# Kernel optimization log

Measured on AMD Instinct MI355X. Metric: run time of the kernel, lower is better.

The kernel has to match this reference:

```python
import jax, jax.numpy as jnp
import numpy as np

N, E, D, H, HD, DFF = 2048, 32768, 256, 8, 32, 1024
NEG = -1e30  # masked-out logit (exp -> 0 in fp32)


def _layer_norm(x, w, b, eps=1e-5):
    mu = jnp.mean(x, axis=-1, keepdims=True)
    var = jnp.mean((x - mu) ** 2, axis=-1, keepdims=True)
    return (x - mu) * jax.lax.rsqrt(var + eps) * w + b


def setup_inputs() -> dict:
    key = jax.random.key(0)
    ks = jax.random.split(key, 24)
    w = lambda k, shape: (jax.random.normal(k, shape, dtype=jnp.float32) * 0.02)
    inp = {
        "node_feat": jax.random.normal(ks[0], (N, D), dtype=jnp.float32),
        "edge_feat": jax.random.normal(ks[1], (E, 10), dtype=jnp.float32),
        "src": jax.random.randint(ks[2], (E,), 0, N),
        "dst": jax.random.randint(ks[3], (E,), 0, N),
        "Wq": w(ks[4], (D, D)), "bq": jnp.zeros((D,), jnp.float32),
        "Wk": w(ks[5], (D, D)), "bk": jnp.zeros((D,), jnp.float32),
        "Wv": w(ks[6], (D, D)), "bv": jnp.zeros((D,), jnp.float32),
        "Wo": w(ks[7], (D, D)), "bo": jnp.zeros((D,), jnp.float32),
        "We": w(ks[8], (10, H)), "be": jnp.zeros((H,), jnp.float32),
        "n1w": jnp.ones((D,), jnp.float32), "n1b": jnp.zeros((D,), jnp.float32),
        "W1": w(ks[9], (D, DFF)), "b1": jnp.zeros((DFF,), jnp.float32),
        "W2": w(ks[10], (DFF, D)), "b2": jnp.zeros((D,), jnp.float32),
        "n2w": jnp.ones((D,), jnp.float32), "n2b": jnp.zeros((D,), jnp.float32),
    }
    return inp


def reference(node_feat, edge_feat, src, dst, Wq, bq, Wk, bk, Wv, bv, Wo, bo,
              We, be, n1w, n1b, W1, b1, W2, b2, n2w, n2b):
    n = node_feat.shape[0]
    Q = (node_feat @ Wq + bq).reshape(n, H, HD)
    K = (node_feat @ Wk + bk).reshape(n, H, HD)
    V = (node_feat @ Wv + bv).reshape(n, H, HD)

    # dense [n, n, H] scores (faithful to the original dense blowup)
    scores = jnp.einsum('ihd,jhd->ijh', Q, K) / np.sqrt(HD).astype(np.float32)

    # scatter edge bias into dense matrix (last-write semantics like torch indexing)
    edge_bias = edge_feat @ We + be                       # [E, H]
    bias = jnp.zeros((n, n, H), jnp.float32).at[src, dst].set(edge_bias)
    scores = scores + bias

    # symmetric adjacency mask with self-loops
    adj = jnp.zeros((n, n), jnp.float32)
    adj = adj.at[src, dst].set(1.0).at[dst, src].set(1.0)
    idx = jnp.arange(n)
    adj = adj.at[idx, idx].set(1.0)

    scores = jnp.where(adj[:, :, None] > 0, scores, NEG)
    attn = jax.nn.softmax(scores, axis=1)                 # softmax over j (dim=1)

    out = jnp.einsum('ijh,jhd->ihd', attn, V).reshape(n, D)
    out = out @ Wo + bo
    out = _layer_norm(out + node_feat, n1w, n1b)
    ffn = jax.nn.relu(out @ W1 + b1) @ W2 + b2
    out = _layer_norm(out + ffn, n2w, n2b)
    return out
```

## Files before the change

### kernel.cpp

```cpp
#include <hip/hip_runtime.h>
#include <hip/hip_bf16.h>

#define NN 2048
#define E_CNT 32768
#define D 256
#define DFF 1024
#define MAXN 256
#define NCONV 14

typedef __hip_bfloat16 bf16;
typedef __attribute__((ext_vector_type(8))) short short8;
typedef __attribute__((ext_vector_type(4))) float f32x4;

__device__ __forceinline__ short bf2s(bf16 x) { union { bf16 b; short s; } u; u.b = x; return u.s; }
__device__ __forceinline__ float bs2f(unsigned short v) { return __uint_as_float(((unsigned)v) << 16); }

struct ConvTab { const void* src[NCONV]; int n[NCONV]; int off[NCONV]; };
struct TransTab { const void* src[6]; int K[6]; int N[6]; int off[6]; };

__global__ __launch_bounds__(256) void k_sniff(const unsigned short* __restrict__ p,
                                               int* __restrict__ flagp)
{
    int tid = threadIdx.x;
    int cnt = 0;
    for (int t = tid; t < 2048; t += 256) {
        float f = __uint_as_float(((unsigned)p[t]) << 16);
        if (!(fabsf(f) < 1000.f)) cnt++;
    }
#pragma unroll
    for (int off = 32; off > 0; off >>= 1) cnt += __shfl_down(cnt, off, 64);
    __shared__ int s[4];
    if ((tid & 63) == 0) s[tid >> 6] = cnt;
    __syncthreads();
    if (tid == 0) *flagp = (s[0] + s[1] + s[2] + s[3] > 64) ? 1 : 0;
}

__global__ __launch_bounds__(256) void k_convert(ConvTab tab, float* __restrict__ base,
                                                 bf16* __restrict__ nb,
                                                 const void* __restrict__ nodesrc,
                                                 const int* __restrict__ flagp)
{
    int a = blockIdx.y;
    int flag = *flagp;
    int idx0 = blockIdx.x * 2048 + threadIdx.x;
    if (a == NCONV) {
        const int n = NN * D;
        if (flag) {
            const float* s = (const float*)nodesrc;
#pragma unroll
            for (int k = 0; k < 8; k++) { int i = idx0 + k * 256; if (i < n) nb[i] = __float2bfloat16(s[i]); }
        } else {
            const short* s = (const short*)nodesrc;
            short* d = (short*)nb;
#pragma unroll
            for (int k = 0; k < 8; k++) { int i = idx0 + k * 256; if (i < n) d[i] = s[i]; }
        }
        return;
    }
    int n = tab.n[a];
    const void* s = tab.src[a];
    float* d = base + tab.off[a];
    if (flag) {
        const float* sf = (const float*)s;
#pragma unroll
        for (int k = 0; k < 8; k++) { int i = idx0 + k * 256; if (i < n) d[i] = sf[i]; }
    } else {
        const bf16* sb = (const bf16*)s;
#pragma unroll
        for (int k = 0; k < 8; k++) { int i = idx0 + k * 256; if (i < n) d[i] = __bfloat162float(sb[i]); }
    }
}

__global__ __launch_bounds__(256) void k_trans(TransTab tab, short* __restrict__ wt,
                                               const int* __restrict__ flagp)
{
    int a = blockIdx.z;
    int Kd = tab.K[a], Nd = tab.N[a];
    int n0 = blockIdx.x * 32, k0 = blockIdx.y * 32;
    if (n0 >= Nd || k0 >= Kd) return;
    int flag = *flagp;
    __shared__ short tile[32][33];
    int t = threadIdx.x, c = t & 31, r4 = t >> 5;
    const void* s = tab.src[a];
#pragma unroll
    for (int p = 0; p < 4; p++) {
        int r = r4 + p * 8;
        short v;
        if (flag) v = bf2s(__float2bfloat16(((const float*)s)[(size_t)(k0 + r) * Nd + n0 + c]));
        else      v = ((const short*)s)[(size_t)(k0 + r) * Nd + n0 + c];
        tile[r][c] = v;
    }
    __syncthreads();
    short* dT = wt + tab.off[a];
#pragma unroll
    for (int p = 0; p < 4; p++) {
        int r = r4 + p * 8;
        dT[(size_t)(n0 + r) * Kd + k0 + c] = tile[c][r];
    }
}

__global__ __launch_bounds__(256) void k_fill_edge(
    const int* __restrict__ src, const int* __restrict__ dst,
    int* __restrict__ pair, unsigned* __restrict__ bits,
    const float* __restrict__ ef, const float* __restrict__ We,
    const float* __restrict__ be, float* __restrict__ ebuf)
{
    __shared__ float w[80], bb[8];
    int tid = threadIdx.x;
    int e = blockIdx.x * 256 + tid;
    if (blockIdx.y == 0) {
        if (e < E_CNT) {
            int s = src[e], d = dst[e];
            atomicMax(&pair[(size_t)s * NN + d], e);
            atomicOr(&bits[s * 64 + (d >> 5)], 1u << (d & 31));
            atomicOr(&bits[d * 64 + (s >> 5)], 1u << (s & 31));
        }
        if (e < NN) atomicOr(&bits[e * 64 + (e >> 5)], 1u << (e & 31));
        return;
    }
    if (tid < 80) w[tid] = We[tid];
    if (tid < 8)  bb[tid] = be[tid];
    __syncthreads();
    if (e < E_CNT) {
        float v[10];
#pragma unroll
        for (int t2 = 0; t2 < 10; t2++) v[t2] = ef[e * 10 + t2];
#pragma unroll
        for (int h = 0; h < 8; h++) {
            float s = bb[h];
#pragma unroll
            for (int t2 = 0; t2 < 10; t2++) s += v[t2] * w[t2 * 8 + h];
            ebuf[e * 8 + h] = s;
        }
    }
}

__global__ __launch_bounds__(256) void k_qkv3(
    const bf16* __restrict__ A,
    const bf16* __restrict__ WqT, const bf16* __restrict__ WkT, const bf16* __restrict__ WvT,
    const float* __restrict__ bq, const float* __restrict__ bk, const float* __restrict__ bv,
    float* __restrict__ Qo, bf16* __restrict__ Kb, bf16* __restrict__ Vb)
{
    int z = blockIdx.z;
    const bf16* BT = (z == 0) ? WqT : (z == 1) ? WkT : WvT;
    const float* bias = (z == 0) ? bq : (z == 1) ? bk : bv;
    __shared__ __align__(16) short As[2][4 * 64 * 8];
    __shared__ __align__(16) short Bs[2][4 * 32 * 8];
    int t = threadIdx.x, w = t >> 6, l = t & 63, fr = l & 15, fc = l >> 4;
    int i0 = blockIdx.x * 64, j0 = blockIdx.y * 32;
    int lr = t >> 2, lc = t & 3;
    f32x4 acc0 = {0.f, 0.f, 0.f, 0.f}, acc1 = {0.f, 0.f, 0.f, 0.f};
    const short* ap = (const short*)A + (size_t)(i0 + lr) * D + lc * 8;
    const short* bp = (const short*)BT + (size_t)(j0 + (lr & 31)) * D + lc * 8;
    for (int k0 = 0; k0 < D; k0 += 64) {
        short8 av0 = *(const short8*)(ap + k0);
        short8 av1 = *(const short8*)(ap + k0 + 32);
        short8 bv0 = {}, bv1 = {};
        if (t < 128) {
            bv0 = *(const short8*)(bp + k0);
            bv1 = *(const short8*)(bp + k0 + 32);
        }
        __syncthreads();
        *(short8*)&As[0][(lc * 64 + lr) * 8] = av0;
        *(short8*)&As[1][(lc * 64 + lr) * 8] = av1;
        if (t < 128) {
            *(short8*)&Bs[0][(lc * 32 + lr) * 8] = bv0;
            *(short8*)&Bs[1][(lc * 32 + lr) * 8] = bv1;
        }
        __syncthreads();
#pragma unroll
        for (int s = 0; s < 2; s++) {
            short8 af  = *(const short8*)&As[s][(fc * 64 + w * 16 + fr) * 8];
            short8 bf0 = *(const short8*)&Bs[s][(fc * 32 + fr) * 8];
            short8 bf1 = *(const short8*)&Bs[s][(fc * 32 + 16 + fr) * 8];
            acc0 = __builtin_amdgcn_mfma_f32_16x16x32_bf16(af, bf0, acc0, 0, 0, 0);
            acc1 = __builtin_amdgcn_mfma_f32_16x16x32_bf16(af, bf1, acc1, 0, 0, 0);
        }
    }
    float bb0 = bias[j0 + fr], bb1 = bias[j0 + 16 + fr];
    int orow = i0 + w * 16 + fc * 4;
    if (z == 0) {
#pragma unroll
        for (int j = 0; j < 4; j++) {
            Qo[(size_t)(orow + j) * D + j0 + fr]      = acc0[j] + bb0;
            Qo[(size_t)(orow + j) * D + j0 + 16 + fr] = acc1[j] + bb1;
        }
    } else {
        bf16* C = (z == 1) ? Kb : Vb;
#pragma unroll
        for (int j = 0; j < 4; j++) {
            C[(size_t)(orow + j) * D + j0 + fr]      = __float2bfloat16(acc0[j] + bb0);
            C[(size_t)(orow + j) * D + j0 + 16 + fr] = __float2bfloat16(acc1[j] + bb1);
        }
    }
}

template<int EPI>
__global__ __launch_bounds__(256) void k_gemm(
    const bf16* __restrict__ A, const bf16* __restrict__ BT,
    const float* __restrict__ bias, void* __restrict__ Cp, int N, int K)
{
    __shared__ __align__(16) short As[2][4 * 64 * 8];
    __shared__ __align__(16) short Bs[2][4 * 32 * 8];
    int t = threadIdx.x;
    int w = t >> 6, l = t & 63;
    int fr = l & 15, fc = l >> 4;
    int i0 = blockIdx.x * 64, j0 = blockIdx.y * 32;
    int lr = t >> 2, lc = t & 3;
    f32x4 acc0 = {0.f, 0.f, 0.f, 0.f}, acc1 = {0.f, 0.f, 0.f, 0.f};
    const short* ap = (const short*)A + (size_t)(i0 + lr) * K + lc * 8;
    const short* bp = (const short*)BT + (size_t)(j0 + (lr & 31)) * K + lc * 8;
    for (int k0 = 0; k0 < K; k0 += 64) {
        short8 av0 = *(const short8*)(ap + k0);
        short8 av1 = *(const short8*)(ap + k0 + 32);
        short8 bv0 = {}, bv1 = {};
        if (t < 128) {
            bv0 = *(const short8*)(bp + k0);
            bv1 = *(const short8*)(bp + k0 + 32);
        }
        __syncthreads();
        *(short8*)&As[0][(lc * 64 + lr) * 8] = av0;
        *(short8*)&As[1][(lc * 64 + lr) * 8] = av1;
        if (t < 128) {
            *(short8*)&Bs[0][(lc * 32 + lr) * 8] = bv0;
            *(short8*)&Bs[1][(lc * 32 + lr) * 8] = bv1;
        }
        __syncthreads();
#pragma unroll
        for (int s = 0; s < 2; s++) {
            short8 af  = *(const short8*)&As[s][(fc * 64 + w * 16 + fr) * 8];
            short8 bf0 = *(const short8*)&Bs[s][(fc * 32 + fr) * 8];
            short8 bf1 = *(const short8*)&Bs[s][(fc * 32 + 16 + fr) * 8];
            acc0 = __builtin_amdgcn_mfma_f32_16x16x32_bf16(af, bf0, acc0, 0, 0, 0);
            acc1 = __builtin_amdgcn_mfma_f32_16x16x32_bf16(af, bf1, acc1, 0, 0, 0);
        }
    }
    float bb0 = bias[j0 + fr];
    float bb1 = bias[j0 + 16 + fr];
    int orow = i0 + w * 16 + fc * 4;
    if (EPI == 0) {
        float* C = (float*)Cp;
#pragma unroll
        for (int j = 0; j < 4; j++) {
            C[(size_t)(orow + j) * N + j0 + fr]      = acc0[j] + bb0;
            C[(size_t)(orow + j) * N + j0 + 16 + fr] = acc1[j] + bb1;
        }
    } else {
        bf16* C = (bf16*)Cp;
#pragma unroll
        for (int j = 0; j < 4; j++) {
            C[(size_t)(orow + j) * N + j0 + fr]      = __float2bfloat16(fmaxf(acc0[j] + bb0, 0.f));
            C[(size_t)(orow + j) * N + j0 + 16 + fr] = __float2bfloat16(fmaxf(acc1[j] + bb1, 0.f));
        }
    }
}

__global__ __launch_bounds__(256) void k_attn(
    const float* __restrict__ Q, const bf16* __restrict__ K,
    const bf16* __restrict__ V, const float* __restrict__ eb,
    const int* __restrict__ pair, const unsigned* __restrict__ bits,
    bf16* __restrict__ attn_out)
{
    int i = blockIdx.x;
    int tid = threadIdx.x;
    __shared__ float q[D];
    __shared__ int   nbr[MAXN];
    __shared__ int   eid[MAXN];
    __shared__ float sc[MAXN][8];
    __shared__ float mh[8], lhi[8];
    __shared__ int   nn_s;
    q[tid] = Q[(size_t)i * D + tid];
    if (tid < 64) {
        unsigned wrd = bits[i * 64 + tid];
        int cnt = __popc(wrd);
        int pre = cnt;
#pragma unroll
        for (int off = 1; off < 64; off <<= 1) {
            int v = __shfl_up(pre, off, 64);
            if (tid >= off) pre += v;
        }
        int pos = pre - cnt;
        while (wrd) {
            int b = __ffs(wrd) - 1;
            wrd &= wrd - 1;
            if (pos < MAXN) nbr[pos] = tid * 32 + b;
            pos++;
        }
        if (tid == 63) nn_s = (pre < MAXN) ? pre : MAXN;
    }
    __syncthreads();
    int nn = nn_s;
    const size_t prow = (size_t)i * NN;
    for (int n = tid; n < nn; n += 256) eid[n] = pair[prow + nbr[n]];
    __syncthreads();
    const short* Ks = (const short*)K;
    for (int t2 = tid; t2 < nn * 8; t2 += 256) {
        int n = t2 >> 3, h = t2 & 7;
        int j = nbr[n];
        const short8* kr = (const short8*)(Ks + (size_t)j * D + h * 32);
        const float4* qr = (const float4*)(q + h * 32);
        float s = 0.f;
#pragma unroll
        for (int c = 0; c < 4; c++) {
            short8 kv = kr[c];
            float4 q0 = qr[c * 2], q1 = qr[c * 2 + 1];
            s += q0.x * bs2f((unsigned short)kv[0]) + q0.y * bs2f((unsigned short)kv[1])
               + q0.z * bs2f((unsigned short)kv[2]) + q0.w * bs2f((unsigned short)kv[3])
               + q1.x * bs2f((unsigned short)kv[4]) + q1.y * bs2f((unsigned short)kv[5])
               + q1.z * bs2f((unsigned short)kv[6]) + q1.w * bs2f((unsigned short)kv[7]);
        }
        s *= 0.17677669529663687f;
        int e = eid[n];
        if (e >= 0) s += eb[e * 8 + h];
        sc[n][h] = s;
    }
    __syncthreads();
    {
        int h = tid >> 5, l32 = tid & 31;
        float m = -1e30f;
        for (int n = l32; n < nn; n += 32) m = fmaxf(m, sc[n][h]);
#pragma unroll
        for (int off = 1; off < 32; off <<= 1) m = fmaxf(m, __shfl_xor(m, off, 64));
        float lsum = 0.f;
        for (int n = l32; n < nn; n += 32) lsum += __expf(sc[n][h] - m);
#pragma unroll
        for (int off = 1; off < 32; off <<= 1) lsum += __shfl_xor(lsum, off, 64);
        if (l32 == 0) { mh[h] = m; lhi[h] = 1.f / lsum; }
    }
    __syncthreads();
    for (int t2 = tid; t2 < nn * 8; t2 += 256) {
        int n = t2 >> 3, h = t2 & 7;
        sc[n][h] = __expf(sc[n][h] - mh[h]);
    }
    __syncthreads();
    int h = tid >> 5;
    const unsigned short* Vu = (const unsigned short*)V;
    float acc = 0.f;
    int n = 0;
    for (; n + 4 <= nn; n += 4) {
        int j0 = nbr[n], j1 = nbr[n + 1], j2 = nbr[n + 2], j3 = nbr[n + 3];
        float p0 = sc[n][h], p1 = sc[n + 1][h], p2 = sc[n + 2][h], p3 = sc[n + 3][h];
        acc += p0 * bs2f(Vu[(size_t)j0 * D + tid]) + p1 * bs2f(Vu[(size_t)j1 * D + tid])
             + p2 * bs2f(Vu[(size_t)j2 * D + tid]) + p3 * bs2f(Vu[(size_t)j3 * D + tid]);
    }
    for (; n < nn; n++) acc += sc[n][h] * bs2f(Vu[(size_t)nbr[n] * D + tid]);
    attn_out[(size_t)i * D + tid] = __float2bfloat16(acc * lhi[h]);
}

template<int MODE>
__global__ __launch_bounds__(256) void k_ln(
    const float* __restrict__ g, const float* __restrict__ res,
    const float* __restrict__ w, const float* __restrict__ b,
    float* __restrict__ xf, bf16* __restrict__ xb, const int* __restrict__ flagp)
{
    int row = blockIdx.x * 4 + (threadIdx.x >> 6);
    int l = threadIdx.x & 63;
    size_t base = (size_t)row * D + l * 4;
    float4 gv = *(const float4*)(g + base);
    float4 rv = *(const float4*)(res + base);
    float v0 = gv.x + rv.x, v1 = gv.y + rv.y, v2 = gv.z + rv.z, v3 = gv.w + rv.w;
    float s = v0 + v1 + v2 + v3;
    float q = v0 * v0 + v1 * v1 + v2 * v2 + v3 * v3;
#pragma unroll
    for (int off = 32; off > 0; off >>= 1) {
        s += __shfl_xor(s, off, 64);
        q += __shfl_xor(q, off, 64);
    }
    float mu  = s * (1.f / D);
    float var = q * (1.f / D) - mu * mu;
    float rs  = rsqrtf(var + 1e-5f);
    float4 wv = *(const float4*)(w + l * 4);
    float4 bv = *(const float4*)(b + l * 4);
    float o0 = (v0 - mu) * rs * wv.x + bv.x;
    float o1 = (v1 - mu) * rs * wv.y + bv.y;
    float o2 = (v2 - mu) * rs * wv.z + bv.z;
    float o3 = (v3 - mu) * rs * wv.w + bv.w;
    if (MODE == 0) {
        float4 o; o.x = o0; o.y = o1; o.z = o2; o.w = o3;
        *(float4*)(xf + base) = o;
        xb[base + 0] = __float2bfloat16(o0);
        xb[base + 1] = __float2bfloat16(o1);
        xb[base + 2] = __float2bfloat16(o2);
        xb[base + 3] = __float2bfloat16(o3);
    } else {
        if (*flagp) {
            float4 o; o.x = o0; o.y = o1; o.z = o2; o.w = o3;
            *(float4*)(xf + base) = o;
        } else {
            xb[base + 0] = __float2bfloat16(o0);
            xb[base + 1] = __float2bfloat16(o1);
            xb[base + 2] = __float2bfloat16(o2);
            xb[base + 3] = __float2bfloat16(o3);
        }
    }
}

extern "C" void kernel_launch(void* const* d_in, const int* in_sizes, int n_in,
                              void* d_out, int out_size, void* d_ws, size_t ws_size,
                              hipStream_t stream)
{
    (void)n_in; (void)out_size; (void)ws_size;
    const int* src = (const int*)d_in[2];
    const int* dst = (const int*)d_in[3];

    char* ws = (char*)d_ws;
    const size_t KB = 1024;
    float*    conv     = (float*)ws;
    bf16*     node_b16 = (bf16*)(ws + 3584 * KB);
    short*    wt       = (short*)(ws + 4608 * KB);
    int*      flagp    = (int*)(ws + 6144 * KB);
    unsigned* bits     = (unsigned*)(ws + 6272 * KB);
    float*    eb       = (float*)(ws + 7168 * KB);
    float*    Q        = (float*)(ws + 8192 * KB);
    bf16*     Kb       = (bf16*)(ws + 10240 * KB);
    bf16*     Vb       = (bf16*)(ws + 11264 * KB);
    bf16*     attn_out = (bf16*)(ws + 12288 * KB);
    float*    x1f      = (float*)(ws + 13312 * KB);
    bf16*     x1b      = (bf16*)(ws + 15360 * KB);
    int*      pair     = (int*)(ws + 16384 * KB);
    float*    g2       = (float*)(ws + 32768 * KB);
    bf16*     hid      = (bf16*)(ws + 34816 * KB);
    float*    g4       = (float*)(ws + 38912 * KB);

    static const int conv_idx[NCONV] = {0, 1, 5, 7, 9, 11, 12, 13, 14, 15, 17, 19, 20, 21};
    ConvTab tab;
    int off = 0;
    for (int a = 0; a < NCONV; a++) {
        int gi = conv_idx[a];
        tab.src[a] = d_in[gi];
        tab.n[a]   = in_sizes[gi];
        tab.off[a] = off;
        off += (in_sizes[gi] + 255) & ~255;
    }
    const float* node_f32 = conv + tab.off[0];
    const float* edge_f32 = conv + tab.off[1];
    const float* fbq  = conv + tab.off[2];
    const float* fbk  = conv + tab.off[3];
    const float* fbv  = conv + tab.off[4];
    const float* fbo  = conv + tab.off[5];
    const float* fWe  = conv + tab.off[6];
    const float* fbe  = conv + tab.off[7];
    const float* fn1w = conv + tab.off[8];
    const float* fn1b = conv + tab.off[9];
    const float* fb1  = conv + tab.off[10];
    const float* fb2  = conv + tab.off[11];
    const float* fn2w = conv + tab.off[12];
    const float* fn2b = conv + tab.off[13];

    TransTab tt;
    const int widx[6] = {4, 6, 8, 10, 16, 18};
    const int wK[6] = {256, 256, 256, 256, 256, 1024};
    const int wN[6] = {256, 256, 256, 256, 1024, 256};
    const int woff[6] = {0, 65536, 131072, 196608, 262144, 524288};
    for (int a = 0; a < 6; a++) { tt.src[a] = d_in[widx[a]]; tt.K[a] = wK[a]; tt.N[a] = wN[a]; tt.off[a] = woff[a]; }
    const bf16* WqT = (const bf16*)(wt + 0);
    const bf16* WkT = (const bf16*)(wt + 65536);
    const bf16* WvT = (const bf16*)(wt + 131072);
    const bf16* WoT = (const bf16*)(wt + 196608);
    const bf16* W1T = (const bf16*)(wt + 262144);
    const bf16* W2T = (const bf16*)(wt + 524288);

    hipMemsetAsync(bits, 0x00, (size_t)NN * 64 * 4, stream);
    hipMemsetAsync(pair, 0xFF, (size_t)NN * NN * 4, stream);

    k_sniff<<<1, 256, 0, stream>>>((const unsigned short*)d_in[0], flagp);
    k_convert<<<dim3(256, NCONV + 1), 256, 0, stream>>>(tab, conv, node_b16, d_in[0], flagp);
    k_trans<<<dim3(32, 32, 6), 256, 0, stream>>>(tt, wt, flagp);
    k_fill_edge<<<dim3(128, 2), 256, 0, stream>>>(src, dst, pair, bits,
                                                  edge_f32, fWe, fbe, eb);
    k_qkv3<<<dim3(32, 8, 3), 256, 0, stream>>>(node_b16, WqT, WkT, WvT, fbq, fbk, fbv, Q, Kb, Vb);
    k_attn<<<NN, 256, 0, stream>>>(Q, Kb, Vb, eb, pair, bits, attn_out);

    k_gemm<0><<<dim3(32, 8), 256, 0, stream>>>(attn_out, WoT, fbo, g2, D, D);
    k_ln<0><<<NN / 4, 256, 0, stream>>>(g2, node_f32, fn1w, fn1b, x1f, x1b, flagp);
    k_gemm<1><<<dim3(32, 32), 256, 0, stream>>>(x1b, W1T, fb1, hid, DFF, D);
    k_gemm<0><<<dim3(32, 8), 256, 0, stream>>>(hid, W2T, fb2, g4, D, DFF);
    k_ln<1><<<NN / 4, 256, 0, stream>>>(g4, x1f, fn2w, fn2b, (float*)d_out, (bf16*)d_out, flagp);
}
```

Before: 167.3 us.

## Merge prep kernels, fuse GEMM with LayerNorm, store Q in bf16

```diff
diff --git a/kernel.cpp b/kernel.cpp
--- a/kernel.cpp
+++ b/kernel.cpp
@@ -6,7 +6,6 @@
 #define D 256
 #define DFF 1024
 #define MAXN 256
-#define NCONV 14
 
 typedef __hip_bfloat16 bf16;
 typedef __attribute__((ext_vector_type(8))) short short8;
@@ -15,122 +14,145 @@
 __device__ __forceinline__ short bf2s(bf16 x) { union { bf16 b; short s; } u; u.b = x; return u.s; }
 __device__ __forceinline__ float bs2f(unsigned short v) { return __uint_as_float(((unsigned)v) << 16); }
 
-struct ConvTab { const void* src[NCONV]; int n[NCONV]; int off[NCONV]; };
-struct TransTab { const void* src[6]; int K[6]; int N[6]; int off[6]; };
-
-__global__ __launch_bounds__(256) void k_sniff(const unsigned short* __restrict__ p,
-                                               int* __restrict__ flagp)
+__device__ __forceinline__ int sniff_flag(const unsigned short* p, int* sh)
 {
     int tid = threadIdx.x;
     int cnt = 0;
-    for (int t = tid; t < 2048; t += 256) {
-        float f = __uint_as_float(((unsigned)p[t]) << 16);
+    for (int t = tid; t < 512; t += 256) {
+        float f = bs2f(p[t]);
         if (!(fabsf(f) < 1000.f)) cnt++;
     }
 #pragma unroll
     for (int off = 32; off > 0; off >>= 1) cnt += __shfl_down(cnt, off, 64);
-    __shared__ int s[4];
-    if ((tid & 63) == 0) s[tid >> 6] = cnt;
+    if ((tid & 63) == 0) sh[tid >> 6] = cnt;
     __syncthreads();
-    if (tid == 0) *flagp = (s[0] + s[1] + s[2] + s[3] > 64) ? 1 : 0;
-}
-
-__global__ __launch_bounds__(256) void k_convert(ConvTab tab, float* __restrict__ base,
-                                                 bf16* __restrict__ nb,
-                                                 const void* __restrict__ nodesrc,
-                                                 const int* __restrict__ flagp)
-{
-    int a = blockIdx.y;
-    int flag = *flagp;
-    int idx0 = blockIdx.x * 2048 + threadIdx.x;
-    if (a == NCONV) {
-        const int n = NN * D;
+    int tot = sh[0] + sh[1] + sh[2] + sh[3];
+    return tot > 16;
+}
+
+struct PrepArgs {
+    const void* node; const void* edge;
+    const int* src; const int* dst;
+    const void* We; const void* be;
+    const void* wsrc[6];
+    const void* ssrc[10]; int sn[10]; int soff[10];
+    bf16* node_b16; float* node_f32; float* smalls;
+    short* wt; float* eb; int* pair; unsigned* bits;
+    int* flagp;
+};
+
+__global__ __launch_bounds__(256) void k_prep(PrepArgs A)
+{
+    __shared__ int sh[4];
+    __shared__ short tile[32][33];
+    __shared__ float wsm[80], bbs[8];
+    const int b = blockIdx.x;
+    const int t = threadIdx.x;
+
+    if (b >= 1408 && b < 1536) {
+        int e = (b - 1408) * 256 + t;
+        if (e < E_CNT) {
+            int s = A.src[e], d = A.dst[e];
+            atomicMax(&A.pair[(size_t)s * NN + d], e);
+            atomicOr(&A.bits[s * 64 + (d >> 5)], 1u << (d & 31));
+            atomicOr(&A.bits[d * 64 + (s >> 5)], 1u << (s & 31));
+        }
+        int n = (b - 1408) * 16 + (t >> 4);
+        if (t < 128 && n < NN) atomicOr(&A.bits[n * 64 + (n >> 5)], 1u << (n & 31));
+        return;
+    }
+
+    const int flag = sniff_flag((const unsigned short*)A.node, sh);
+
+    if (b < 768) {
+        int a, ti, ntn;
+        if (b < 256)      { a = b >> 6; ti = b & 63;  ntn = 8;  }
+        else if (b < 512) { a = 4;      ti = b - 256; ntn = 32; }
+        else              { a = 5;      ti = b - 512; ntn = 8;  }
+        const int Kd = (a == 5) ? 1024 : 256;
+        const int Nd = (a == 4) ? 1024 : 256;
+        int n0 = (ti % ntn) * 32, k0 = (ti / ntn) * 32;
+        const void* s = A.wsrc[a];
+        int c = t & 31, r4 = t >> 5;
+#pragma unroll
+        for (int p = 0; p < 4; p++) {
+            int r = r4 + p * 8;
+            short v;
+            if (flag) v = bf2s(__float2bfloat16(((const float*)s)[(size_t)(k0 + r) * Nd + n0 + c]));
+            else      v = ((const short*)s)[(size_t)(k0 + r) * Nd + n0 + c];
+            tile[r][c] = v;
+        }
+        __syncthreads();
+        static const int woff[6] = {0, 65536, 131072, 196608, 262144, 524288};
+        short* dT = A.wt + woff[a];
+#pragma unroll
+        for (int p = 0; p < 4; p++) {
+            int r = r4 + p * 8;
+            dT[(size_t)(n0 + r) * Kd + k0 + c] = tile[c][r];
+        }
+        return;
+    }
+    if (b < 1024) {
+        int i0 = (b - 768) * 2048 + t;
         if (flag) {
-            const float* s = (const float*)nodesrc;
-#pragma unroll
-            for (int k = 0; k < 8; k++) { int i = idx0 + k * 256; if (i < n) nb[i] = __float2bfloat16(s[i]); }
+            const float* s = (const float*)A.node;
+#pragma unroll
+            for (int k = 0; k < 8; k++) A.node_b16[i0 + k * 256] = __float2bfloat16(s[i0 + k * 256]);
         } else {
-            const short* s = (const short*)nodesrc;
-            short* d = (short*)nb;
-#pragma unroll
-            for (int k = 0; k < 8; k++) { int i = idx0 + k * 256; if (i < n) d[i] = s[i]; }
+            const short* s = (const short*)A.node;
+            short* d = (short*)A.node_b16;
+#pragma unroll
+            for (int k = 0; k < 8; k++) d[i0 + k * 256] = s[i0 + k * 256];
         }
         return;
     }
-    int n = tab.n[a];
-    const void* s = tab.src[a];
-    float* d = base + tab.off[a];
-    if (flag) {
-        const float* sf = (const float*)s;
-#pragma unroll
-        for (int k = 0; k < 8; k++) { int i = idx0 + k * 256; if (i < n) d[i] = sf[i]; }
-    } else {
-        const bf16* sb = (const bf16*)s;
-#pragma unroll
-        for (int k = 0; k < 8; k++) { int i = idx0 + k * 256; if (i < n) d[i] = __bfloat162float(sb[i]); }
-    }
-}
-
-__global__ __launch_bounds__(256) void k_trans(TransTab tab, short* __restrict__ wt,
-                                               const int* __restrict__ flagp)
-{
-    int a = blockIdx.z;
-    int Kd = tab.K[a], Nd = tab.N[a];
-    int n0 = blockIdx.x * 32, k0 = blockIdx.y * 32;
-    if (n0 >= Nd || k0 >= Kd) return;
-    int flag = *flagp;
-    __shared__ short tile[32][33];
-    int t = threadIdx.x, c = t & 31, r4 = t >> 5;
-    const void* s = tab.src[a];
-#pragma unroll
-    for (int p = 0; p < 4; p++) {
-        int r = r4 + p * 8;
-        short v;
-        if (flag) v = bf2s(__float2bfloat16(((const float*)s)[(size_t)(k0 + r) * Nd + n0 + c]));
-        else      v = ((const short*)s)[(size_t)(k0 + r) * Nd + n0 + c];
-        tile[r][c] = v;
-    }
-    __syncthreads();
-    short* dT = wt + tab.off[a];
-#pragma unroll
-    for (int p = 0; p < 4; p++) {
-        int r = r4 + p * 8;
-        dT[(size_t)(n0 + r) * Kd + k0 + c] = tile[c][r];
-    }
-}
-
-__global__ __launch_bounds__(256) void k_fill_edge(
-    const int* __restrict__ src, const int* __restrict__ dst,
-    int* __restrict__ pair, unsigned* __restrict__ bits,
-    const float* __restrict__ ef, const float* __restrict__ We,
-    const float* __restrict__ be, float* __restrict__ ebuf)
-{
-    __shared__ float w[80], bb[8];
-    int tid = threadIdx.x;
-    int e = blockIdx.x * 256 + tid;
-    if (blockIdx.y == 0) {
-        if (e < E_CNT) {
-            int s = src[e], d = dst[e];
-            atomicMax(&pair[(size_t)s * NN + d], e);
-            atomicOr(&bits[s * 64 + (d >> 5)], 1u << (d & 31));
-            atomicOr(&bits[d * 64 + (s >> 5)], 1u << (s & 31));
-        }
-        if (e < NN) atomicOr(&bits[e * 64 + (e >> 5)], 1u << (e & 31));
+    if (b < 1280) {
+        int i0 = (b - 1024) * 2048 + t;
+        if (flag) {
+            const float* s = (const float*)A.node;
+#pragma unroll
+            for (int k = 0; k < 8; k++) A.node_f32[i0 + k * 256] = s[i0 + k * 256];
+        } else {
+            const bf16* s = (const bf16*)A.node;
+#pragma unroll
+            for (int k = 0; k < 8; k++) A.node_f32[i0 + k * 256] = __bfloat162float(s[i0 + k * 256]);
+        }
         return;
     }
-    if (tid < 80) w[tid] = We[tid];
-    if (tid < 8)  bb[tid] = be[tid];
-    __syncthreads();
-    if (e < E_CNT) {
+    if (b < 1408) {
+        if (t < 80) wsm[t] = flag ? ((const float*)A.We)[t] : __bfloat162float(((const bf16*)A.We)[t]);
+        if (t < 8)  bbs[t] = flag ? ((const float*)A.be)[t] : __bfloat162float(((const bf16*)A.be)[t]);
+        __syncthreads();
+        int e = (b - 1280) * 256 + t;
         float v[10];
-#pragma unroll
-        for (int t2 = 0; t2 < 10; t2++) v[t2] = ef[e * 10 + t2];
+        if (flag) {
+            const float* ef = (const float*)A.edge;
+#pragma unroll
+            for (int k = 0; k < 10; k++) v[k] = ef[e * 10 + k];
+        } else {
+            const bf16* ef = (const bf16*)A.edge;
+#pragma unroll
+            for (int k = 0; k < 10; k++) v[k] = __bfloat162float(ef[e * 10 + k]);
+        }
 #pragma unroll
         for (int h = 0; h < 8; h++) {
-            float s = bb[h];
-#pragma unroll
-            for (int t2 = 0; t2 < 10; t2++) s += v[t2] * w[t2 * 8 + h];
-            ebuf[e * 8 + h] = s;
+            float s = bbs[h];
+#pragma unroll
+            for (int k = 0; k < 10; k++) s += v[k] * wsm[k * 8 + h];
+            A.eb[e * 8 + h] = s;
+        }
+        return;
+    }
+    if (t == 0) *A.flagp = flag;
+    for (int a = 0; a < 10; a++) {
+        int n = A.sn[a];
+        float* d = A.smalls + A.soff[a];
+        if (flag) {
+            const float* s = (const float*)A.ssrc[a];
+            for (int i = t; i < n; i += 256) d[i] = s[i];
+        } else {
+            const bf16* s = (const bf16*)A.ssrc[a];
+            for (int i = t; i < n; i += 256) d[i] = __bfloat162float(s[i]);
         }
     }
 }
@@ -139,11 +161,12 @@
     const bf16* __restrict__ A,
     const bf16* __restrict__ WqT, const bf16* __restrict__ WkT, const bf16* __restrict__ WvT,
     const float* __restrict__ bq, const float* __restrict__ bk, const float* __restrict__ bv,
-    float* __restrict__ Qo, bf16* __restrict__ Kb, bf16* __restrict__ Vb)
+    bf16* __restrict__ Qb, bf16* __restrict__ Kb, bf16* __restrict__ Vb)
 {
     int z = blockIdx.z;
     const bf16* BT = (z == 0) ? WqT : (z == 1) ? WkT : WvT;
     const float* bias = (z == 0) ? bq : (z == 1) ? bk : bv;
+    bf16* C = (z == 0) ? Qb : (z == 1) ? Kb : Vb;
     __shared__ __align__(16) short As[2][4 * 64 * 8];
     __shared__ __align__(16) short Bs[2][4 * 32 * 8];
     int t = threadIdx.x, w = t >> 6, l = t & 63, fr = l & 15, fc = l >> 4;
@@ -179,19 +202,10 @@
     }
     float bb0 = bias[j0 + fr], bb1 = bias[j0 + 16 + fr];
     int orow = i0 + w * 16 + fc * 4;
-    if (z == 0) {
-#pragma unroll
-        for (int j = 0; j < 4; j++) {
-            Qo[(size_t)(orow + j) * D + j0 + fr]      = acc0[j] + bb0;
-            Qo[(size_t)(orow + j) * D + j0 + 16 + fr] = acc1[j] + bb1;
-        }
-    } else {
-        bf16* C = (z == 1) ? Kb : Vb;
-#pragma unroll
-        for (int j = 0; j < 4; j++) {
-            C[(size_t)(orow + j) * D + j0 + fr]      = __float2bfloat16(acc0[j] + bb0);
-            C[(size_t)(orow + j) * D + j0 + 16 + fr] = __float2bfloat16(acc1[j] + bb1);
-        }
+#pragma unroll
+    for (int j = 0; j < 4; j++) {
+        C[(size_t)(orow + j) * D + j0 + fr]      = __float2bfloat16(acc0[j] + bb0);
+        C[(size_t)(orow + j) * D + j0 + 16 + fr] = __float2bfloat16(acc1[j] + bb1);
     }
 }
 
@@ -238,25 +252,16 @@
     float bb0 = bias[j0 + fr];
     float bb1 = bias[j0 + 16 + fr];
     int orow = i0 + w * 16 + fc * 4;
-    if (EPI == 0) {
-        float* C = (float*)Cp;
-#pragma unroll
-        for (int j = 0; j < 4; j++) {
-            C[(size_t)(orow + j) * N + j0 + fr]      = acc0[j] + bb0;
-            C[(size_t)(orow + j) * N + j0 + 16 + fr] = acc1[j] + bb1;
-        }
-    } else {
-        bf16* C = (bf16*)Cp;
-#pragma unroll
-        for (int j = 0; j < 4; j++) {
-            C[(size_t)(orow + j) * N + j0 + fr]      = __float2bfloat16(fmaxf(acc0[j] + bb0, 0.f));
-            C[(size_t)(orow + j) * N + j0 + 16 + fr] = __float2bfloat16(fmaxf(acc1[j] + bb1, 0.f));
-        }
+    bf16* C = (bf16*)Cp;
+#pragma unroll
+    for (int j = 0; j < 4; j++) {
+        C[(size_t)(orow + j) * N + j0 + fr]      = __float2bfloat16(fmaxf(acc0[j] + bb0, 0.f));
+        C[(size_t)(orow + j) * N + j0 + 16 + fr] = __float2bfloat16(fmaxf(acc1[j] + bb1, 0.f));
     }
 }
 
 __global__ __launch_bounds__(256) void k_attn(
-    const float* __restrict__ Q, const bf16* __restrict__ K,
+    const bf16* __restrict__ Q, const bf16* __restrict__ K,
     const bf16* __restrict__ V, const float* __restrict__ eb,
     const int* __restrict__ pair, const unsigned* __restrict__ bits,
     bf16* __restrict__ attn_out)
@@ -267,9 +272,9 @@
     __shared__ int   nbr[MAXN];
     __shared__ int   eid[MAXN];
     __shared__ float sc[MAXN][8];
-    __shared__ float mh[8], lhi[8];
+    __shared__ float lhi[8];
     __shared__ int   nn_s;
-    q[tid] = Q[(size_t)i * D + tid];
+    q[tid] = bs2f(((const unsigned short*)Q)[(size_t)i * D + tid]);
     if (tid < 64) {
         unsigned wrd = bits[i * 64 + tid];
         int cnt = __popc(wrd);
@@ -322,15 +327,14 @@
 #pragma unroll
         for (int off = 1; off < 32; off <<= 1) m = fmaxf(m, __shfl_xor(m, off, 64));
         float lsum = 0.f;
-        for (int n = l32; n < nn; n += 32) lsum += __expf(sc[n][h] - m);
+        for (int n = l32; n < nn; n += 32) {
+            float e = __expf(sc[n][h] - m);
+            sc[n][h] = e;
+            lsum += e;
+        }
 #pragma unroll
         for (int off = 1; off < 32; off <<= 1) lsum += __shfl_xor(lsum, off, 64);
-        if (l32 == 0) { mh[h] = m; lhi[h] = 1.f / lsum; }
-    }
-    __syncthreads();
-    for (int t2 = tid; t2 < nn * 8; t2 += 256) {
-        int n = t2 >> 3, h = t2 & 7;
-        sc[n][h] = __expf(sc[n][h] - mh[h]);
+        if (l32 == 0) lhi[h] = 1.f / lsum;
     }
     __syncthreads();
     int h = tid >> 5;
@@ -347,50 +351,97 @@
     attn_out[(size_t)i * D + tid] = __float2bfloat16(acc * lhi[h]);
 }
 
-template<int MODE>
-__global__ __launch_bounds__(256) void k_ln(
-    const float* __restrict__ g, const float* __restrict__ res,
-    const float* __restrict__ w, const float* __restrict__ b,
-    float* __restrict__ xf, bf16* __restrict__ xb, const int* __restrict__ flagp)
-{
-    int row = blockIdx.x * 4 + (threadIdx.x >> 6);
-    int l = threadIdx.x & 63;
-    size_t base = (size_t)row * D + l * 4;
-    float4 gv = *(const float4*)(g + base);
-    float4 rv = *(const float4*)(res + base);
-    float v0 = gv.x + rv.x, v1 = gv.y + rv.y, v2 = gv.z + rv.z, v3 = gv.w + rv.w;
-    float s = v0 + v1 + v2 + v3;
-    float q = v0 * v0 + v1 * v1 + v2 * v2 + v3 * v3;
-#pragma unroll
-    for (int off = 32; off > 0; off >>= 1) {
-        s += __shfl_xor(s, off, 64);
-        q += __shfl_xor(q, off, 64);
+template<int MODE, int KDIM>
+__global__ __launch_bounds__(256) void k_gemmln(
+    const bf16* __restrict__ A, const bf16* __restrict__ BT,
+    const float* __restrict__ bias, const float* __restrict__ res,
+    const float* __restrict__ lnw, const float* __restrict__ lnb,
+    float* __restrict__ outf, bf16* __restrict__ outb, const int* __restrict__ flagp)
+{
+    __shared__ __align__(16) short As[4 * 32 * 8];
+    __shared__ __align__(16) short Bs[4 * 256 * 8];
+    __shared__ float Cs[32][257];
+    int t = threadIdx.x;
+    int w = t >> 6, l = t & 63, fr = l & 15, fc = l >> 4;
+    int i0 = blockIdx.x * 32;
+    int ar = t >> 2, akc = t & 3;
+    f32x4 acc[2][4];
+#pragma unroll
+    for (int rt = 0; rt < 2; rt++)
+#pragma unroll
+        for (int c = 0; c < 4; c++) acc[rt][c] = {0.f, 0.f, 0.f, 0.f};
+    const short* ap = (const short*)A + (size_t)(i0 + (ar & 31)) * KDIM + akc * 8;
+    const short* bp = (const short*)BT;
+    short8 av = {};
+    if (t < 128) av = *(const short8*)(ap);
+    short8 bv[4];
+#pragma unroll
+    for (int p = 0; p < 4; p++)
+        bv[p] = *(const short8*)(bp + (size_t)(p * 64 + ar) * KDIM + akc * 8);
+    for (int k0 = 0; k0 < KDIM; k0 += 32) {
+        __syncthreads();
+        if (t < 128) *(short8*)&As[(akc * 32 + ar) * 8] = av;
+#pragma unroll
+        for (int p = 0; p < 4; p++)
+            *(short8*)&Bs[(akc * 256 + p * 64 + ar) * 8] = bv[p];
+        __syncthreads();
+        if (k0 + 32 < KDIM) {
+            if (t < 128) av = *(const short8*)(ap + k0 + 32);
+#pragma unroll
+            for (int p = 0; p < 4; p++)
+                bv[p] = *(const short8*)(bp + (size_t)(p * 64 + ar) * KDIM + k0 + 32 + akc * 8);
+        }
+        short8 af0 = *(const short8*)&As[(fc * 32 + fr) * 8];
+        short8 af1 = *(const short8*)&As[(fc * 32 + 16 + fr) * 8];
+#pragma unroll
+        for (int c = 0; c < 4; c++) {
+            int ct = w * 4 + c;
+            short8 bfr = *(const short8*)&Bs[(fc * 256 + ct * 16 + fr) * 8];
+            acc[0][c] = __builtin_amdgcn_mfma_f32_16x16x32_bf16(af0, bfr, acc[0][c], 0, 0, 0);
+            acc[1][c] = __builtin_amdgcn_mfma_f32_16x16x32_bf16(af1, bfr, acc[1][c], 0, 0, 0);
+        }
+    }
+#pragma unroll
+    for (int rt = 0; rt < 2; rt++)
+#pragma unroll
+        for (int c = 0; c < 4; c++) {
+            int ct = w * 4 + c;
+            float bb = bias[ct * 16 + fr];
+#pragma unroll
+            for (int j = 0; j < 4; j++)
+                Cs[rt * 16 + fc * 4 + j][ct * 16 + fr] = acc[rt][c][j] + bb;
+        }
+    __syncthreads();
+    int r = t >> 3, c0 = t & 7;
+    float vbuf[32];
+    float s = 0.f, qq = 0.f;
+#pragma unroll
+    for (int m = 0; m < 32; m++) {
+        int c = c0 + m * 8;
+        float v = Cs[r][c] + res[(size_t)(i0 + r) * D + c];
+        vbuf[m] = v;
+        s += v; qq += v * v;
+    }
+#pragma unroll
+    for (int off = 1; off < 8; off <<= 1) {
+        s  += __shfl_xor(s, off, 64);
+        qq += __shfl_xor(qq, off, 64);
     }
     float mu  = s * (1.f / D);
-    float var = q * (1.f / D) - mu * mu;
-    float rs  = rsqrtf(var + 1e-5f);
-    float4 wv = *(const float4*)(w + l * 4);
-    float4 bv = *(const float4*)(b + l * 4);
-    float o0 = (v0 - mu) * rs * wv.x + bv.x;
-    float o1 = (v1 - mu) * rs * wv.y + bv.y;
-    float o2 = (v2 - mu) * rs * wv.z + bv.z;
-    float o3 = (v3 - mu) * rs * wv.w + bv.w;
-    if (MODE == 0) {
-        float4 o; o.x = o0; o.y = o1; o.z = o2; o.w = o3;
-        *(float4*)(xf + base) = o;
-        xb[base + 0] = __float2bfloat16(o0);
-        xb[base + 1] = __float2bfloat16(o1);
-        xb[base + 2] = __float2bfloat16(o2);
-        xb[base + 3] = __float2bfloat16(o3);
-    } else {
-        if (*flagp) {
-            float4 o; o.x = o0; o.y = o1; o.z = o2; o.w = o3;
-            *(float4*)(xf + base) = o;
+    float var = qq * (1.f / D) - mu * mu;
+    float rsd = rsqrtf(var + 1e-5f);
+    int flag = (MODE == 1) ? *flagp : 0;
+#pragma unroll
+    for (int m = 0; m < 32; m++) {
+        int c = c0 + m * 8;
+        float o = (vbuf[m] - mu) * rsd * lnw[c] + lnb[c];
+        size_t idx = (size_t)(i0 + r) * D + c;
+        if (MODE == 0) {
+            outf[idx] = o;
+            outb[idx] = __float2bfloat16(o);
         } else {
-            xb[base + 0] = __float2bfloat16(o0);
-            xb[base + 1] = __float2bfloat16(o1);
-            xb[base + 2] = __float2bfloat16(o2);
-            xb[base + 3] = __float2bfloat16(o3);
+            if (flag) outf[idx] = o;
+            else      outb[idx] = __float2bfloat16(o);
         }
     }
 }
@@ -399,9 +450,7 @@
                               void* d_out, int out_size, void* d_ws, size_t ws_size,
                               hipStream_t stream)
 {
-    (void)n_in; (void)out_size; (void)ws_size;
-    const int* src = (const int*)d_in[2];
-    const int* dst = (const int*)d_in[3];
+    (void)in_sizes; (void)n_in; (void)out_size; (void)ws_size;
 
     char* ws = (char*)d_ws;
     const size_t KB = 1024;
@@ -411,48 +460,33 @@
     int*      flagp    = (int*)(ws + 6144 * KB);
     unsigned* bits     = (unsigned*)(ws + 6272 * KB);
     float*    eb       = (float*)(ws + 7168 * KB);
-    float*    Q        = (float*)(ws + 8192 * KB);
+    bf16*     Qb       = (bf16*)(ws + 8192 * KB);
     bf16*     Kb       = (bf16*)(ws + 10240 * KB);
     bf16*     Vb       = (bf16*)(ws + 11264 * KB);
     bf16*     attn_out = (bf16*)(ws + 12288 * KB);
     float*    x1f      = (float*)(ws + 13312 * KB);
     bf16*     x1b      = (bf16*)(ws + 15360 * KB);
     int*      pair     = (int*)(ws + 16384 * KB);
-    float*    g2       = (float*)(ws + 32768 * KB);
     bf16*     hid      = (bf16*)(ws + 34816 * KB);
-    float*    g4       = (float*)(ws + 38912 * KB);
-
-    static const int conv_idx[NCONV] = {0, 1, 5, 7, 9, 11, 12, 13, 14, 15, 17, 19, 20, 21};
-    ConvTab tab;
-    int off = 0;
-    for (int a = 0; a < NCONV; a++) {
-        int gi = conv_idx[a];
-        tab.src[a] = d_in[gi];
-        tab.n[a]   = in_sizes[gi];
-        tab.off[a] = off;
-        off += (in_sizes[gi] + 255) & ~255;
-    }
-    const float* node_f32 = conv + tab.off[0];
-    const float* edge_f32 = conv + tab.off[1];
-    const float* fbq  = conv + tab.off[2];
-    const float* fbk  = conv + tab.off[3];
-    const float* fbv  = conv + tab.off[4];
-    const float* fbo  = conv + tab.off[5];
-    const float* fWe  = conv + tab.off[6];
-    const float* fbe  = conv + tab.off[7];
-    const float* fn1w = conv + tab.off[8];
-    const float* fn1b = conv + tab.off[9];
-    const float* fb1  = conv + tab.off[10];
-    const float* fb2  = conv + tab.off[11];
-    const float* fn2w = conv + tab.off[12];
-    const float* fn2b = conv + tab.off[13];
-
-    TransTab tt;
-    const int widx[6] = {4, 6, 8, 10, 16, 18};
-    const int wK[6] = {256, 256, 256, 256, 256, 1024};
-    const int wN[6] = {256, 256, 256, 256, 1024, 256};
-    const int woff[6] = {0, 65536, 131072, 196608, 262144, 524288};
-    for (int a = 0; a < 6; a++) { tt.src[a] = d_in[widx[a]]; tt.K[a] = wK[a]; tt.N[a] = wN[a]; tt.off[a] = woff[a]; }
+
+    float* node_f32 = conv;
+    float* smalls   = conv + 524288;
+    static const int sidx[10] = {5, 7, 9, 11, 14, 15, 17, 19, 20, 21};
+    static const int ssz[10]  = {256, 256, 256, 256, 256, 256, 1024, 256, 256, 256};
+    int soff[10]; int so = 0;
+    for (int a = 0; a < 10; a++) { soff[a] = so; so += ssz[a]; }
+    const float* fbq  = smalls + soff[0];
+    const float* fbk  = smalls + soff[1];
+    const float* fbv  = smalls + soff[2];
+    const float* fbo  = smalls + soff[3];
+    const float* fn1w = smalls + soff[4];
+    const float* fn1b = smalls + soff[5];
+    const float* fb1  = smalls + soff[6];
+    const float* fb2  = smalls + soff[7];
+    const float* fn2w = smalls + soff[8];
+    const float* fn2b = smalls + soff[9];
+
+    static const int widx[6] = {4, 6, 8, 10, 16, 18};
     const bf16* WqT = (const bf16*)(wt + 0);
     const bf16* WkT = (const bf16*)(wt + 65536);
     const bf16* WvT = (const bf16*)(wt + 131072);
@@ -460,20 +494,24 @@
     const bf16* W1T = (const bf16*)(wt + 262144);
     const bf16* W2T = (const bf16*)(wt + 524288);
 
+    PrepArgs pa;
+    pa.node = d_in[0]; pa.edge = d_in[1];
+    pa.src = (const int*)d_in[2]; pa.dst = (const int*)d_in[3];
+    pa.We = d_in[12]; pa.be = d_in[13];
+    for (int a = 0; a < 6; a++)  pa.wsrc[a] = d_in[widx[a]];
+    for (int a = 0; a < 10; a++) { pa.ssrc[a] = d_in[sidx[a]]; pa.sn[a] = ssz[a]; pa.soff[a] = soff[a]; }
+    pa.node_b16 = node_b16; pa.node_f32 = node_f32; pa.smalls = smalls;
+    pa.wt = wt; pa.eb = eb; pa.pair = pair; pa.bits = bits; pa.flagp = flagp;
+
     hipMemsetAsync(bits, 0x00, (size_t)NN * 64 * 4, stream);
     hipMemsetAsync(pair, 0xFF, (size_t)NN * NN * 4, stream);
 
-    k_sniff<<<1, 256, 0, stream>>>((const unsigned short*)d_in[0], flagp);
-    k_convert<<<dim3(256, NCONV + 1), 256, 0, stream>>>(tab, conv, node_b16, d_in[0], flagp);
-    k_trans<<<dim3(32, 32, 6), 256, 0, stream>>>(tt, wt, flagp);
-    k_fill_edge<<<dim3(128, 2), 256, 0, stream>>>(src, dst, pair, bits,
-                                                  edge_f32, fWe, fbe, eb);
-    k_qkv3<<<dim3(32, 8, 3), 256, 0, stream>>>(node_b16, WqT, WkT, WvT, fbq, fbk, fbv, Q, Kb, Vb);
-    k_attn<<<NN, 256, 0, stream>>>(Q, Kb, Vb, eb, pair, bits, attn_out);
-
-    k_gemm<0><<<dim3(32, 8), 256, 0, stream>>>(attn_out, WoT, fbo, g2, D, D);
-    k_ln<0><<<NN / 4, 256, 0, stream>>>(g2, node_f32, fn1w, fn1b, x1f, x1b, flagp);
+    k_prep<<<1537, 256, 0, stream>>>(pa);
+    k_qkv3<<<dim3(32, 8, 3), 256, 0, stream>>>(node_b16, WqT, WkT, WvT, fbq, fbk, fbv, Qb, Kb, Vb);
+    k_attn<<<NN, 256, 0, stream>>>(Qb, Kb, Vb, eb, pair, bits, attn_out);
+    k_gemmln<0, 256><<<64, 256, 0, stream>>>(attn_out, WoT, fbo, node_f32, fn1w, fn1b,
+                                             x1f, x1b, flagp);
     k_gemm<1><<<dim3(32, 32), 256, 0, stream>>>(x1b, W1T, fb1, hid, DFF, D);
-    k_gemm<0><<<dim3(32, 8), 256, 0, stream>>>(hid, W2T, fb2, g4, D, DFF);
-    k_ln<1><<<NN / 4, 256, 0, stream>>>(g4, x1f, fn2w, fn2b, (float*)d_out, (bf16*)d_out, flagp);
-}
+    k_gemmln<1, 1024><<<64, 256, 0, stream>>>(hid, W2T, fb2, x1f, fn2w, fn2b,
+                                              (float*)d_out, (bf16*)d_out, flagp);
+}
```

Result: slower. 171.1 us (+2.3%).
